# Optimization experiments

Hardware: AMD Instinct MI355X
Metric: run time of the kernel (lower is better)

Reference implementation:

```python
import jax, jax.numpy as jnp
import numpy as np

N = 50000      # nodes
E = 800000     # edges per graph (avg degree 16)
F_IN = 256     # input feature dim
H = 64         # hidden dim
K = 32         # number of pure sources / topics
NEG_SLOPE = 0.2


def _add_self_loops(ei, n):
    loop = jnp.arange(n, dtype=ei.dtype)
    return jnp.concatenate([ei, jnp.stack([loop, loop])], axis=1)


def _gatv2(x, ei, Wl, Wr, att, bias, n):
    """PyG GATv2Conv, heads=1: e_ij = att . leaky_relu(Wl x_j + Wr x_i),
    softmax over incoming edges per target i, out_i = sum_j alpha_ij * Wl x_j + bias."""
    src, dst = ei[0], ei[1]            # edge j -> i  (source, target)
    xl = x @ Wl                        # [n, H] source transform (also the message)
    xr = x @ Wr                        # [n, H] target transform
    msg = xl[src]                      # [E, H] gathered source messages
    s = jax.nn.leaky_relu(msg + xr[dst], negative_slope=NEG_SLOPE) @ att  # [E]
    # numerically stable segment softmax over dst
    smax = jax.ops.segment_max(s, dst, num_segments=n)
    ex = jnp.exp(s - smax[dst])
    denom = jax.ops.segment_sum(ex, dst, num_segments=n)
    alpha = ex / (denom[dst] + 1e-16)
    out = jax.ops.segment_sum(msg * alpha[:, None], dst, num_segments=n)
    return out + bias


def setup_inputs() -> dict:
    key = jax.random.key(0)
    ks = jax.random.split(key, 14)
    X = jax.random.normal(ks[0], (N, F_IN), jnp.float32)
    ei_feat = jax.random.randint(ks[1], (2, E), 0, N, dtype=jnp.int64)
    ei_spatial = jax.random.randint(ks[2], (2, E), 0, N, dtype=jnp.int64)
    s1 = 1.0 / np.sqrt(F_IN)
    s2 = 1.0 / np.sqrt(H)
    Wl1 = jax.random.normal(ks[3], (F_IN, H), jnp.float32) * s1
    Wr1 = jax.random.normal(ks[4], (F_IN, H), jnp.float32) * s1
    att1 = jax.random.normal(ks[5], (H,), jnp.float32) * s2
    b1 = jnp.zeros((H,), jnp.float32)
    Wl2 = jax.random.normal(ks[6], (H, K), jnp.float32) * s2
    Wr2 = jax.random.normal(ks[7], (H, K), jnp.float32) * s2
    att2 = jax.random.normal(ks[8], (K,), jnp.float32) * (1.0 / np.sqrt(K))
    b2 = jnp.zeros((K,), jnp.float32)
    M = jax.random.uniform(ks[9], (K, F_IN), jnp.float32)
    edge_w = jax.random.normal(ks[10], (1,), jnp.float32)
    return {"X": X, "ei_feat": ei_feat, "ei_spatial": ei_spatial,
            "Wl1": Wl1, "Wr1": Wr1, "att1": att1, "b1": b1,
            "Wl2": Wl2, "Wr2": Wr2, "att2": att2, "b2": b2,
            "M": M, "edge_w": edge_w}


def reference(X, ei_feat, ei_spatial, Wl1, Wr1, att1, b1, Wl2, Wr2, att2, b2, M, edge_w):
    ei = _add_self_loops(ei_feat, N)
    h = jax.nn.elu(_gatv2(X, ei, Wl1, Wr1, att1, b1, N))          # [N, H]
    Z = jax.nn.softmax(_gatv2(h, ei, Wl2, Wr2, att2, b2, N), axis=1)  # [N, K]
    X_pure = Z @ jax.nn.relu(M)                                   # [N, F]
    row, col = ei_spatial[0], ei_spatial[1]
    w = jax.nn.sigmoid(edge_w)                                    # (1,)
    contam = jax.ops.segment_sum(X_pure[col], row, num_segments=N)  # scatter_add
    return Z, X_pure + w * contam, w
```

## Files before the change

### kernel.cpp

```cpp
#include <hip/hip_runtime.h>
#include <math.h>

#define N_NODES 50000
#define E_EDGES 800000
#define F_INDIM 256
#define H_DIM   64
#define K_DIM   32
#define NEG_SLOPE 0.2f

#define SLOT 64
#define RANGE_N 12500
#define FILL_WGPG 256
#define FILL_SLICE (E_EDGES / FILL_WGPG)

typedef short short8v __attribute__((ext_vector_type(8)));
typedef unsigned short us8 __attribute__((ext_vector_type(8)));
typedef float f32x4 __attribute__((ext_vector_type(4)));

__device__ __forceinline__ unsigned short f2bf(float f) {
    unsigned u = __float_as_uint(f);
    unsigned r = (u + 0x7FFFu + ((u >> 16) & 1u)) >> 16;
    return (unsigned short)r;
}
__device__ __forceinline__ float bf2f(unsigned short h) {
    return __uint_as_float(((unsigned)h) << 16);
}

template<int CTRL>
__device__ __forceinline__ float dpp_xadd(float v) {
    int x = __builtin_amdgcn_update_dpp(0, __float_as_int(v), CTRL, 0xF, 0xF, true);
    return v + __int_as_float(x);
}
template<int CTRL>
__device__ __forceinline__ float dpp_xmax(float v) {
    int x = __builtin_amdgcn_update_dpp(0, __float_as_int(v), CTRL, 0xF, 0xF, true);
    return fmaxf(v, __int_as_float(x));
}
__device__ __forceinline__ float red_sum64(float v) {
    v = dpp_xadd<0xB1>(v); v = dpp_xadd<0x4E>(v);
    v = dpp_xadd<0x141>(v); v = dpp_xadd<0x140>(v);
    v += __shfl_xor(v, 16, 64);
    v += __shfl_xor(v, 32, 64);
    return v;
}
__device__ __forceinline__ float red_sum32(float v) {
    v = dpp_xadd<0xB1>(v); v = dpp_xadd<0x4E>(v);
    v = dpp_xadd<0x141>(v); v = dpp_xadd<0x140>(v);
    v += __shfl_xor(v, 16, 64);
    return v;
}
__device__ __forceinline__ float red_max32(float v) {
    v = dpp_xmax<0xB1>(v); v = dpp_xmax<0x4E>(v);
    v = dpp_xmax<0x141>(v); v = dpp_xmax<0x140>(v);
    v = fmaxf(v, __shfl_xor(v, 16, 64));
    return v;
}

__global__ __launch_bounds__(256) void prep_kernel(
        const float* __restrict__ Wl, const float* __restrict__ Wr,
        unsigned short* __restrict__ Bh, unsigned short* __restrict__ Bl,
        int* __restrict__ curF, int* __restrict__ curS) {
    const int t = blockIdx.x * 256 + threadIdx.x;
    if (t < N_NODES) { curF[t] = t * SLOT; curS[t] = t * SLOT; }
    if (t >= 4096) return;
    const int lane = t & 63;
    const int ks = (t >> 6) & 7;
    const int ct = t >> 9;
    const int n = ct * 16 + (lane & 15);
    const int kbase = ks * 32 + (lane >> 4) * 8;
    const float* W = (n < H_DIM) ? Wl : Wr;
    const int col = n & 63;
#pragma unroll
    for (int e = 0; e < 8; ++e) {
        float w = W[(size_t)(kbase + e) * H_DIM + col];
        unsigned short hi = f2bf(w);
        unsigned short lo = f2bf(w - bf2f(hi));
        Bh[(size_t)t * 8 + e] = hi;
        Bl[(size_t)t * 8 + e] = lo;
    }
}

__global__ __launch_bounds__(256) void gemm1_mfma_kernel(
        const float* __restrict__ X,
        const unsigned short* __restrict__ Bh, const unsigned short* __restrict__ Bl,
        unsigned short* __restrict__ xlb, float* __restrict__ xr) {
    const int wv = threadIdx.x >> 6;
    const int lane = threadIdx.x & 63;
    const int m0 = blockIdx.x * 64 + wv * 16;
    const int r = lane & 15;
    const int g = lane >> 4;
    int arow = m0 + r;
    if (arow > N_NODES - 1) arow = N_NODES - 1;
    const float* xrow = X + (size_t)arow * F_INDIM + g * 8;

    f32x4 acc[8];
#pragma unroll
    for (int c = 0; c < 8; ++c) acc[c] = (f32x4){0.f, 0.f, 0.f, 0.f};

    for (int ks = 0; ks < 8; ++ks) {
        const float4 f0 = *(const float4*)(xrow + ks * 32);
        const float4 f1 = *(const float4*)(xrow + ks * 32 + 4);
        float f[8] = {f0.x, f0.y, f0.z, f0.w, f1.x, f1.y, f1.z, f1.w};
        union { us8 u; short8v s; } Ah, Al;
#pragma unroll
        for (int j = 0; j < 8; ++j) {
            unsigned short hi = f2bf(f[j]);
            Ah.u[j] = hi;
            Al.u[j] = f2bf(f[j] - bf2f(hi));
        }
        union { us8 u; short8v s; } bh[8], bl[8];
#pragma unroll
        for (int ct = 0; ct < 8; ++ct) {
            const size_t fo = ((size_t)(ct * 8 + ks) * 64 + lane) * 8;
            bh[ct].u = *(const us8*)(Bh + fo);
            bl[ct].u = *(const us8*)(Bl + fo);
        }
#pragma unroll
        for (int ct = 0; ct < 8; ++ct)
            acc[ct] = __builtin_amdgcn_mfma_f32_16x16x32_bf16(Ah.s, bh[ct].s, acc[ct], 0, 0, 0);
#pragma unroll
        for (int ct = 0; ct < 8; ++ct)
            acc[ct] = __builtin_amdgcn_mfma_f32_16x16x32_bf16(Ah.s, bl[ct].s, acc[ct], 0, 0, 0);
#pragma unroll
        for (int ct = 0; ct < 8; ++ct)
            acc[ct] = __builtin_amdgcn_mfma_f32_16x16x32_bf16(Al.s, bh[ct].s, acc[ct], 0, 0, 0);
    }
#pragma unroll
    for (int ct = 0; ct < 8; ++ct) {
        const int n = ct * 16 + r;
        const int col = n & 63;
#pragma unroll
        for (int i = 0; i < 4; ++i) {
            const int rr = m0 + g * 4 + i;
            if (rr < N_NODES) {
                if (n < H_DIM) xlb[(size_t)rr * H_DIM + col] = f2bf(acc[ct][i]);
                else           xr[(size_t)rr * H_DIM + col] = acc[ct][i];
            }
        }
    }
}

__global__ __launch_bounds__(256) void fillslot_kernel(
        const int* __restrict__ srcF, const int* __restrict__ dstF,
        const int* __restrict__ colS, const int* __restrict__ rowS,
        int* __restrict__ curF, int* __restrict__ curS,
        int* __restrict__ csrF, int* __restrict__ csrS) {
    const int wg = blockIdx.x;
    const int g  = wg & 7;
    const int j  = wg >> 3;
    const int e0 = j * FILL_SLICE, e1 = e0 + FILL_SLICE;
    const bool feat = (g < 4);
    const int base = (feat ? g : g - 4) * RANGE_N;
    const int* dA = feat ? dstF : rowS;
    const int* sA = feat ? srcF : colS;
    int* cur = feat ? curF : curS;
    int* csr = feat ? csrF : csrS;

    for (int eb = e0 + (int)threadIdx.x; eb < e1; eb += 2048) {
        int d[8], s[8];
        bool ok[8];
#pragma unroll
        for (int k = 0; k < 8; ++k) {
            const int e = eb + k * 256;
            const bool inr = (e < e1);
            const int ee = inr ? e : e0;
            d[k] = __builtin_nontemporal_load(&dA[ee]);
            s[k] = __builtin_nontemporal_load(&sA[ee]);
            ok[k] = inr && ((unsigned)(d[k] - base) < RANGE_N);
        }
        int p[8];
#pragma unroll
        for (int k = 0; k < 8; ++k)
            if (ok[k]) p[k] = atomicAdd(&cur[d[k]], 1);
#pragma unroll
        for (int k = 0; k < 8; ++k)
            if (ok[k] && p[k] < (d[k] + 1) * SLOT) csr[p[k]] = s[k];
    }
}

__global__ __launch_bounds__(256) void agg1_kernel(
        const int* __restrict__ curF, const int* __restrict__ csrF,
        const unsigned short* __restrict__ xlb, const float* __restrict__ xr,
        const float* __restrict__ att1, const float* __restrict__ b1,
        const float* __restrict__ Wl2, const float* __restrict__ Wr2,
        unsigned short* __restrict__ xl2b, float* __restrict__ xr2) {
    __shared__ float hs[4][H_DIM];
    const int wid  = threadIdx.x >> 6;
    const int lane = threadIdx.x & 63;
    const int n = blockIdx.x * 4 + wid;
    const float xrv  = xr[(size_t)n * H_DIM + lane];
    const float attv = att1[lane];
    const int start = n * SLOT;
    const int cnt = min(__builtin_amdgcn_readfirstlane(curF[n]) - start, SLOT) + 1;
    float m = -1e30f, den = 0.f, acc = 0.f;
    int srcs[8];
#pragma unroll
    for (int j = 0; j < 8; ++j) srcs[j] = (j < cnt - 1) ? csrF[start + j] : n;
    for (int t0 = 0; t0 < cnt; t0 += 8) {
        float xc[8];
#pragma unroll
        for (int j = 0; j < 8; ++j) xc[j] = bf2f(xlb[(size_t)srcs[j] * H_DIM + lane]);
        int nsrcs[8];
#pragma unroll
        for (int j = 0; j < 8; ++j) {
            int t = t0 + 8 + j;
            nsrcs[j] = (t < cnt - 1) ? csrF[start + t] : n;
        }
        float v[8];
#pragma unroll
        for (int j = 0; j < 8; ++j) {
            float a = xc[j] + xrv;
            a = a > 0.f ? a : NEG_SLOPE * a;
            v[j] = a * attv;
        }
#pragma unroll
        for (int j = 0; j < 8; ++j) v[j] = red_sum64(v[j]);
        float vmax = -1e30f;
#pragma unroll
        for (int j = 0; j < 8; ++j) {
            if (t0 + j >= cnt) v[j] = -1e30f;
            vmax = fmaxf(vmax, v[j]);
        }
        const float mn = fmaxf(m, vmax);
        const float sc = __expf(m - mn);
        acc *= sc; den *= sc;
#pragma unroll
        for (int j = 0; j < 8; ++j) {
            const float p = __expf(v[j] - mn);
            acc += p * xc[j];
            den += p;
        }
        m = mn;
#pragma unroll
        for (int j = 0; j < 8; ++j) srcs[j] = nsrcs[j];
    }
    float h = acc / den + b1[lane];
    h = h > 0.f ? h : expm1f(h);
    hs[wid][lane] = h;
    __syncthreads();
    const float* W = (lane < K_DIM) ? Wl2 : Wr2;
    const int col = lane & 31;
    float s = 0.f;
#pragma unroll
    for (int k = 0; k < H_DIM; ++k) s += hs[wid][k] * W[k * K_DIM + col];
    if (lane < K_DIM) xl2b[(size_t)n * K_DIM + col] = f2bf(s);
    else              xr2[(size_t)n * K_DIM + col] = s;
}

__global__ __launch_bounds__(256) void agg2_kernel(
        const int* __restrict__ curF, const int* __restrict__ csrF,
        const unsigned short* __restrict__ xl2b, const float* __restrict__ xr2,
        const float* __restrict__ att2, const float* __restrict__ b2,
        float* __restrict__ Z, unsigned short* __restrict__ Zb) {
    const int t = blockIdx.x * 256 + threadIdx.x;
    const int n = t >> 5;
    const int sub = t & 31;
    if (n >= N_NODES) return;
    const float xrv  = xr2[(size_t)n * K_DIM + sub];
    const float attv = att2[sub];
    const int start = n * SLOT;
    const int cnt = min(curF[n] - start, SLOT) + 1;
    float m = -1e30f, den = 0.f, acc = 0.f;
    int srcs[8];
#pragma unroll
    for (int j = 0; j < 8; ++j) srcs[j] = (j < cnt - 1) ? csrF[start + j] : n;
    for (int t0 = 0; t0 < cnt; t0 += 8) {
        float xc[8];
#pragma unroll
        for (int j = 0; j < 8; ++j) xc[j] = bf2f(xl2b[(size_t)srcs[j] * K_DIM + sub]);
        int nsrcs[8];
#pragma unroll
        for (int j = 0; j < 8; ++j) {
            int tt = t0 + 8 + j;
            nsrcs[j] = (tt < cnt - 1) ? csrF[start + tt] : n;
        }
        float v[8];
#pragma unroll
        for (int j = 0; j < 8; ++j) {
            float a = xc[j] + xrv;
            a = a > 0.f ? a : NEG_SLOPE * a;
            v[j] = a * attv;
        }
#pragma unroll
        for (int j = 0; j < 8; ++j) v[j] = red_sum32(v[j]);
        float vmax = -1e30f;
#pragma unroll
        for (int j = 0; j < 8; ++j) {
            if (t0 + j >= cnt) v[j] = -1e30f;
            vmax = fmaxf(vmax, v[j]);
        }
        const float mn = fmaxf(m, vmax);
        const float sc = __expf(m - mn);
        acc *= sc; den *= sc;
#pragma unroll
        for (int j = 0; j < 8; ++j) {
            const float p = __expf(v[j] - mn);
            acc += p * xc[j];
            den += p;
        }
        m = mn;
#pragma unroll
        for (int j = 0; j < 8; ++j) srcs[j] = nsrcs[j];
    }
    float z = acc / den + b2[sub];
    float mx = red_max32(z);
    float e = __expf(z - mx);
    float ssum = red_sum32(e);
    const float zv = e / ssum;
    Z[(size_t)n * K_DIM + sub] = zv;
    Zb[(size_t)n * K_DIM + sub] = f2bf(zv);
}

__global__ __launch_bounds__(256) void saggfinal_kernel(
        const int* __restrict__ curS, const int* __restrict__ csrS,
        const unsigned short* __restrict__ Zb, const float* __restrict__ Z,
        const float* __restrict__ M, const float* __restrict__ edge_w,
        float* __restrict__ out2, float* __restrict__ wout) {
    __shared__ float zs[8][K_DIM];
    const int n0 = blockIdx.x * 8;
    const int tid = threadIdx.x;
    const float w = 1.f / (1.f + __expf(-edge_w[0]));
    {
        const int hw = tid >> 5;
        const int sub = tid & 31;
        const int n = n0 + hw;
        const int start = n * SLOT;
        const int endi = start + min(curS[n] - start, SLOT);
        float acc = 0.f;
        for (int t0 = start; t0 < endi; t0 += 8) {
            float val[8];
#pragma unroll
            for (int j = 0; j < 8; ++j) {
                int tt = t0 + j;
                int c = csrS[tt < endi ? tt : (endi - 1)];
                val[j] = bf2f(Zb[(size_t)c * K_DIM + sub]);
            }
#pragma unroll
            for (int j = 0; j < 8; ++j)
                acc += (t0 + j < endi) ? val[j] : 0.f;
        }
        zs[hw][sub] = Z[(size_t)n * K_DIM + sub] + w * acc;
    }
    __syncthreads();
    float Mr[K_DIM];
#pragma unroll
    for (int k = 0; k < K_DIM; ++k) Mr[k] = fmaxf(M[k * F_INDIM + tid], 0.f);
#pragma unroll
    for (int q = 0; q < 8; ++q) {
        float acc = 0.f;
#pragma unroll
        for (int k = 0; k < K_DIM; ++k) acc += zs[q][k] * Mr[k];
        out2[(size_t)(n0 + q) * F_INDIM + tid] = acc;
    }
    if (n0 == 0 && tid == 0) wout[0] = w;
}

extern "C" void kernel_launch(void* const* d_in, const int* in_sizes, int n_in,
                              void* d_out, int out_size, void* d_ws, size_t ws_size,
                              hipStream_t stream) {
    const float* X    = (const float*)d_in[0];
    const int*   eif  = (const int*)d_in[1];
    const int*   eis  = (const int*)d_in[2];
    const float* Wl1  = (const float*)d_in[3];
    const float* Wr1  = (const float*)d_in[4];
    const float* att1 = (const float*)d_in[5];
    const float* b1   = (const float*)d_in[6];
    const float* Wl2  = (const float*)d_in[7];
    const float* Wr2  = (const float*)d_in[8];
    const float* att2 = (const float*)d_in[9];
    const float* b2   = (const float*)d_in[10];
    const float* M    = (const float*)d_in[11];
    const float* ew   = (const float*)d_in[12];

    const int* srcF = eif;
    const int* dstF = eif + E_EDGES;
    const int* rowS = eis;
    const int* colS = eis + E_EDGES;

    const size_t N = N_NODES;
    char* ws = (char*)d_ws;
    size_t off = 0;
    auto alloc = [&](size_t bytes) { char* p = ws + off; off += (bytes + 255) & ~(size_t)255; return p; };

    unsigned short* xlb = (unsigned short*)alloc(N * H_DIM * sizeof(unsigned short));
    float* xr1  = (float*)alloc(N * H_DIM * sizeof(float));
    unsigned short* xl2b = (unsigned short*)alloc(N * K_DIM * sizeof(unsigned short));
    float* xr2  = (float*)alloc(N * K_DIM * sizeof(float));
    unsigned short* Zb = (unsigned short*)alloc(N * K_DIM * sizeof(unsigned short));
    int*   curF = (int*)alloc(N * sizeof(int));
    int*   curS = (int*)alloc(N * sizeof(int));
    int*   csrF = (int*)alloc((size_t)N * SLOT * sizeof(int));
    int*   csrS = (int*)alloc((size_t)N * SLOT * sizeof(int));
    unsigned short* Bh = (unsigned short*)alloc(4096 * 8 * sizeof(unsigned short));
    unsigned short* Bl = (unsigned short*)alloc(4096 * 8 * sizeof(unsigned short));

    float* Z    = (float*)d_out;
    float* out2 = (float*)d_out + N * (size_t)K_DIM;
    float* wout = (float*)d_out + N * (size_t)(K_DIM + F_INDIM);

    prep_kernel<<<(N_NODES + 255) / 256, 256, 0, stream>>>(Wl1, Wr1, Bh, Bl, curF, curS);
    gemm1_mfma_kernel<<<(N_NODES + 63) / 64, 256, 0, stream>>>(X, Bh, Bl, xlb, xr1);
    fillslot_kernel<<<8 * FILL_WGPG, 256, 0, stream>>>(srcF, dstF, colS, rowS,
                                                       curF, curS, csrF, csrS);

    agg1_kernel<<<N_NODES / 4, 256, 0, stream>>>(curF, csrF, xlb, xr1, att1, b1,
                                                 Wl2, Wr2, xl2b, xr2);
    agg2_kernel<<<(N_NODES * K_DIM + 255) / 256, 256, 0, stream>>>(curF, csrF,
                                                                   xl2b, xr2, att2, b2,
                                                                   Z, Zb);
    saggfinal_kernel<<<N_NODES / 8, 256, 0, stream>>>(curS, csrS, Zb, Z, M, ew, out2, wout);
}
```

Baseline: 230.1 us.

## Build slot CSR with per-range LDS atomic counters instead of global atomics

Replaces the global-atomic slot fill with 32 large workgroups, each owning a 3125-node range and counting in LDS. Each workgroup writes its per-node degrees at the end, so the cursor initialisation in prep_kernel goes away. Each workgroup now scans the whole edge list, and the source index is loaded only for edges in range. The goal is to remove global atomic traffic, at the cost of reading the edges 16 times per graph and using only 32 workgroups.

```diff
diff --git a/kernel.cpp b/kernel.cpp
--- a/kernel.cpp
+++ b/kernel.cpp
@@ -9,9 +9,9 @@
 #define NEG_SLOPE 0.2f
 
 #define SLOT 64
-#define RANGE_N 12500
-#define FILL_WGPG 256
-#define FILL_SLICE (E_EDGES / FILL_WGPG)
+#define NRANGE 16
+#define RANGE_N2 3125
+#define FB 16
 
 typedef short short8v __attribute__((ext_vector_type(8)));
 typedef unsigned short us8 __attribute__((ext_vector_type(8)));
@@ -58,10 +58,8 @@
 
 __global__ __launch_bounds__(256) void prep_kernel(
         const float* __restrict__ Wl, const float* __restrict__ Wr,
-        unsigned short* __restrict__ Bh, unsigned short* __restrict__ Bl,
-        int* __restrict__ curF, int* __restrict__ curS) {
+        unsigned short* __restrict__ Bh, unsigned short* __restrict__ Bl) {
     const int t = blockIdx.x * 256 + threadIdx.x;
-    if (t < N_NODES) { curF[t] = t * SLOT; curS[t] = t * SLOT; }
     if (t >= 4096) return;
     const int lane = t & 63;
     const int ks = (t >> 6) & 7;
@@ -140,46 +138,51 @@
     }
 }
 
-__global__ __launch_bounds__(256) void fillslot_kernel(
+__global__ __launch_bounds__(1024) void ldsfill_kernel(
         const int* __restrict__ srcF, const int* __restrict__ dstF,
         const int* __restrict__ colS, const int* __restrict__ rowS,
-        int* __restrict__ curF, int* __restrict__ curS,
+        int* __restrict__ degF, int* __restrict__ degS,
         int* __restrict__ csrF, int* __restrict__ csrS) {
+    __shared__ int cur_l[RANGE_N2];
     const int wg = blockIdx.x;
-    const int g  = wg & 7;
-    const int j  = wg >> 3;
-    const int e0 = j * FILL_SLICE, e1 = e0 + FILL_SLICE;
-    const bool feat = (g < 4);
-    const int base = (feat ? g : g - 4) * RANGE_N;
+    const bool feat = (wg < NRANGE);
+    const int base = (feat ? wg : wg - NRANGE) * RANGE_N2;
     const int* dA = feat ? dstF : rowS;
     const int* sA = feat ? srcF : colS;
-    int* cur = feat ? curF : curS;
+    int* deg = feat ? degF : degS;
     int* csr = feat ? csrF : csrS;
-
-    for (int eb = e0 + (int)threadIdx.x; eb < e1; eb += 2048) {
-        int d[8], s[8];
-        bool ok[8];
-#pragma unroll
-        for (int k = 0; k < 8; ++k) {
-            const int e = eb + k * 256;
-            const bool inr = (e < e1);
-            const int ee = inr ? e : e0;
+    const int tid = threadIdx.x;
+
+    for (int i = tid; i < RANGE_N2; i += 1024) cur_l[i] = 0;
+    __syncthreads();
+
+    for (int eb = tid; eb < E_EDGES; eb += 1024 * FB) {
+        int d[FB], s[FB];
+        bool ok[FB];
+#pragma unroll
+        for (int k = 0; k < FB; ++k) {
+            const int e = eb + k * 1024;
+            const bool inr = (e < E_EDGES);
+            const int ee = inr ? e : 0;
             d[k] = __builtin_nontemporal_load(&dA[ee]);
-            s[k] = __builtin_nontemporal_load(&sA[ee]);
-            ok[k] = inr && ((unsigned)(d[k] - base) < RANGE_N);
-        }
-        int p[8];
-#pragma unroll
-        for (int k = 0; k < 8; ++k)
-            if (ok[k]) p[k] = atomicAdd(&cur[d[k]], 1);
-#pragma unroll
-        for (int k = 0; k < 8; ++k)
-            if (ok[k] && p[k] < (d[k] + 1) * SLOT) csr[p[k]] = s[k];
-    }
+            ok[k] = inr && ((unsigned)(d[k] - base) < RANGE_N2);
+        }
+#pragma unroll
+        for (int k = 0; k < FB; ++k)
+            if (ok[k]) s[k] = __builtin_nontemporal_load(&sA[eb + k * 1024]);
+#pragma unroll
+        for (int k = 0; k < FB; ++k)
+            if (ok[k]) {
+                int p = atomicAdd(&cur_l[d[k] - base], 1);
+                if (p < SLOT) csr[d[k] * SLOT + p] = s[k];
+            }
+    }
+    __syncthreads();
+    for (int i = tid; i < RANGE_N2; i += 1024) deg[base + i] = cur_l[i];
 }
 
 __global__ __launch_bounds__(256) void agg1_kernel(
-        const int* __restrict__ curF, const int* __restrict__ csrF,
+        const int* __restrict__ degF, const int* __restrict__ csrF,
         const unsigned short* __restrict__ xlb, const float* __restrict__ xr,
         const float* __restrict__ att1, const float* __restrict__ b1,
         const float* __restrict__ Wl2, const float* __restrict__ Wr2,
@@ -191,7 +194,7 @@
     const float xrv  = xr[(size_t)n * H_DIM + lane];
     const float attv = att1[lane];
     const int start = n * SLOT;
-    const int cnt = min(__builtin_amdgcn_readfirstlane(curF[n]) - start, SLOT) + 1;
+    const int cnt = min(__builtin_amdgcn_readfirstlane(degF[n]), SLOT) + 1;
     float m = -1e30f, den = 0.f, acc = 0.f;
     int srcs[8];
 #pragma unroll
@@ -248,7 +251,7 @@
 }
 
 __global__ __launch_bounds__(256) void agg2_kernel(
-        const int* __restrict__ curF, const int* __restrict__ csrF,
+        const int* __restrict__ degF, const int* __restrict__ csrF,
         const unsigned short* __restrict__ xl2b, const float* __restrict__ xr2,
         const float* __restrict__ att2, const float* __restrict__ b2,
         float* __restrict__ Z, unsigned short* __restrict__ Zb) {
@@ -259,7 +262,7 @@
     const float xrv  = xr2[(size_t)n * K_DIM + sub];
     const float attv = att2[sub];
     const int start = n * SLOT;
-    const int cnt = min(curF[n] - start, SLOT) + 1;
+    const int cnt = min(degF[n], SLOT) + 1;
     float m = -1e30f, den = 0.f, acc = 0.f;
     int srcs[8];
 #pragma unroll
@@ -312,7 +315,7 @@
 }
 
 __global__ __launch_bounds__(256) void saggfinal_kernel(
-        const int* __restrict__ curS, const int* __restrict__ csrS,
+        const int* __restrict__ degS, const int* __restrict__ csrS,
         const unsigned short* __restrict__ Zb, const float* __restrict__ Z,
         const float* __restrict__ M, const float* __restrict__ edge_w,
         float* __restrict__ out2, float* __restrict__ wout) {
@@ -325,7 +328,7 @@
         const int sub = tid & 31;
         const int n = n0 + hw;
         const int start = n * SLOT;
-        const int endi = start + min(curS[n] - start, SLOT);
+        const int endi = start + min(degS[n], SLOT);
         float acc = 0.f;
         for (int t0 = start; t0 < endi; t0 += 8) {
             float val[8];
@@ -387,8 +390,8 @@
     unsigned short* xl2b = (unsigned short*)alloc(N * K_DIM * sizeof(unsigned short));
     float* xr2  = (float*)alloc(N * K_DIM * sizeof(float));
     unsigned short* Zb = (unsigned short*)alloc(N * K_DIM * sizeof(unsigned short));
-    int*   curF = (int*)alloc(N * sizeof(int));
-    int*   curS = (int*)alloc(N * sizeof(int));
+    int*   degF = (int*)alloc(N * sizeof(int));
+    int*   degS = (int*)alloc(N * sizeof(int));
     int*   csrF = (int*)alloc((size_t)N * SLOT * sizeof(int));
     int*   csrS = (int*)alloc((size_t)N * SLOT * sizeof(int));
     unsigned short* Bh = (unsigned short*)alloc(4096 * 8 * sizeof(unsigned short));
@@ -398,15 +401,15 @@
     float* out2 = (float*)d_out + N * (size_t)K_DIM;
     float* wout = (float*)d_out + N * (size_t)(K_DIM + F_INDIM);
 
-    prep_kernel<<<(N_NODES + 255) / 256, 256, 0, stream>>>(Wl1, Wr1, Bh, Bl, curF, curS);
+    prep_kernel<<<16, 256, 0, stream>>>(Wl1, Wr1, Bh, Bl);
     gemm1_mfma_kernel<<<(N_NODES + 63) / 64, 256, 0, stream>>>(X, Bh, Bl, xlb, xr1);
-    fillslot_kernel<<<8 * FILL_WGPG, 256, 0, stream>>>(srcF, dstF, colS, rowS,
-                                                       curF, curS, csrF, csrS);
-
-    agg1_kernel<<<N_NODES / 4, 256, 0, stream>>>(curF, csrF, xlb, xr1, att1, b1,
+    ldsfill_kernel<<<2 * NRANGE, 1024, 0, stream>>>(srcF, dstF, colS, rowS,
+                                                    degF, degS, csrF, csrS);
+
+    agg1_kernel<<<N_NODES / 4, 256, 0, stream>>>(degF, csrF, xlb, xr1, att1, b1,
                                                  Wl2, Wr2, xl2b, xr2);
-    agg2_kernel<<<(N_NODES * K_DIM + 255) / 256, 256, 0, stream>>>(curF, csrF,
+    agg2_kernel<<<(N_NODES * K_DIM + 255) / 256, 256, 0, stream>>>(degF, csrF,
                                                                    xl2b, xr2, att2, b2,
                                                                    Z, Zb);
-    saggfinal_kernel<<<N_NODES / 8, 256, 0, stream>>>(curS, csrS, Zb, Z, M, ew, out2, wout);
-}
+    saggfinal_kernel<<<N_NODES / 8, 256, 0, stream>>>(degS, csrS, Zb, Z, M, ew, out2, wout);
+}
```

Result: slower. 371.5 us (+61.5%).
